# Kernel tuning notes

Measured on AMD Instinct MI355X. Metric: run time of the kernel, lower is better.

## Reference

```python
import jax, jax.numpy as jnp
import numpy as np
import math

NUM_HEADS = 16
HEAD_DIM = 64
EMBED = NUM_HEADS * HEAD_DIM  # 1024
T_FEAT = 128


def setup_inputs() -> dict:
    key = jax.random.key(0)
    ks = jax.random.split(key, 9)
    B, S = 4, 2048
    x = jax.random.normal(ks[0], (B, S, EMBED), dtype=jnp.float32)
    time_enc = jax.random.normal(ks[1], (B, T_FEAT), dtype=jnp.float32)
    s = 1.0 / math.sqrt(EMBED)
    Wq = jax.random.normal(ks[2], (EMBED, EMBED), dtype=jnp.float32) * s
    Wk = jax.random.normal(ks[3], (EMBED, EMBED), dtype=jnp.float32) * s
    Wv = jax.random.normal(ks[4], (EMBED, EMBED), dtype=jnp.float32) * s
    Wo = jax.random.normal(ks[5], (EMBED, EMBED), dtype=jnp.float32) * s
    bo = jnp.zeros((EMBED,), dtype=jnp.float32)
    Wt = jax.random.normal(ks[6], (T_FEAT, NUM_HEADS), dtype=jnp.float32) * (1.0 / math.sqrt(T_FEAT))
    bt = jnp.zeros((NUM_HEADS,), dtype=jnp.float32)
    return {"x": x, "time_enc": time_enc, "Wq": Wq, "Wk": Wk, "Wv": Wv,
            "Wo": Wo, "bo": bo, "Wt": Wt, "bt": bt}


def reference(x, time_enc, Wq, Wk, Wv, Wo, bo, Wt, bt):
    B, S, E = x.shape
    H, D = NUM_HEADS, HEAD_DIM
    scale = 1.0 / math.sqrt(D)
    # projections (no bias on q/k/v, bias on out)
    q = (x @ Wq).reshape(B, S, H, D).transpose(0, 2, 1, 3)  # [B,H,S,D]
    k = (x @ Wk).reshape(B, S, H, D).transpose(0, 2, 1, 3)
    v = (x @ Wv).reshape(B, S, H, D).transpose(0, 2, 1, 3)
    scores = jnp.einsum('bhqd,bhkd->bhqk', q, k) * scale
    # time-dependent per-head weighting (softmax over heads)
    time_weights = jax.nn.softmax(time_enc @ Wt + bt)  # [B,H]
    scores = scores * time_weights.reshape(B, H, 1, 1)
    attn = jax.nn.softmax(scores, axis=-1)
    out = jnp.einsum('bhqk,bhkd->bhqd', attn, v)
    out = out.transpose(0, 2, 1, 3).reshape(B, S, E)
    return out @ Wo + bo
```

## Files before the change

kernel.cpp:

```cpp
#include <hip/hip_runtime.h>
#include <cstdint>
#include <cstddef>

#define EMB   1024
#define NH    16
#define HD    64
#define SEQ   2048
#define NB    4
#define MROWS 8192

typedef short short8 __attribute__((ext_vector_type(8)));
typedef float floatx4 __attribute__((ext_vector_type(4)));

__device__ __forceinline__ unsigned short f2bf(float f) {
  return (unsigned short)((__float_as_uint(f) + 0x8000u) >> 16);
}

__device__ __forceinline__ void load16_lds(const unsigned short* g, unsigned short* l) {
  __builtin_amdgcn_global_load_lds((const __attribute__((address_space(1))) void*)g,
                                   (__attribute__((address_space(3))) void*)l, 16, 0, 0);
}

__global__ void time_weights_kernel(const float* __restrict__ te, const float* __restrict__ Wt,
                                    const float* __restrict__ bt, float* __restrict__ tw) {
  int t = threadIdx.x;
  int b = t >> 4, h = t & 15;
  float acc = bt[h];
  for (int i = 0; i < 128; i++) acc += te[b * 128 + i] * Wt[i * 16 + h];
  float m = acc;
  for (int off = 1; off < 16; off <<= 1) m = fmaxf(m, __shfl_xor(m, off, 16));
  float e = __expf(acc - m);
  float s = e;
  for (int off = 1; off < 16; off <<= 1) s += __shfl_xor(s, off, 16);
  tw[t] = (e / s) * 0.125f * 1.4426950408889634f;
}

__global__ void convert_x_kernel(const float4* __restrict__ x, unsigned short* __restrict__ out) {
  int i = blockIdx.x * blockDim.x + threadIdx.x;
  float4 v = x[i];
  unsigned int u0 = __float_as_uint(v.x) + 0x8000u, u1 = __float_as_uint(v.y) + 0x8000u;
  unsigned int u2 = __float_as_uint(v.z) + 0x8000u, u3 = __float_as_uint(v.w) + 0x8000u;
  uint2 p;
  p.x = (u0 >> 16) | (u1 & 0xffff0000u);
  p.y = (u2 >> 16) | (u3 & 0xffff0000u);
  *(uint2*)&out[(size_t)i * 4] = p;
}

__global__ void transpose_convert4_kernel(const float* __restrict__ Wq, const float* __restrict__ Wk,
                                          const float* __restrict__ Wv, const float* __restrict__ Wo,
                                          unsigned short* __restrict__ wqkvt, unsigned short* __restrict__ wot) {
  __shared__ float tile[32][33];
  int z = blockIdx.z;
  const float* W = (z == 0) ? Wq : (z == 1) ? Wk : (z == 2) ? Wv : Wo;
  unsigned short* out = (z < 3) ? (wqkvt + (size_t)z * EMB * EMB) : wot;
  int k0 = blockIdx.x * 32;
  int n0 = blockIdx.y * 32;
  int tx = threadIdx.x;
  int ty = threadIdx.y;
#pragma unroll
  for (int i = 0; i < 4; i++) {
    int k = ty + i * 8;
    tile[k][tx] = W[(size_t)(k0 + k) * EMB + n0 + tx];
  }
  __syncthreads();
#pragma unroll
  for (int i = 0; i < 4; i++) {
    int n = ty + i * 8;
    out[(size_t)(n0 + n) * EMB + k0 + tx] = f2bf(tile[tx][n]);
  }
}

template <int EPI>
__global__ __launch_bounds__(256) void gemm_kernel(
    const unsigned short* __restrict__ A, const unsigned short* __restrict__ Bt,
    unsigned short* __restrict__ qo, unsigned short* __restrict__ ko, unsigned short* __restrict__ vto,
    float* __restrict__ outf, const float* __restrict__ bias, const float* __restrict__ tw) {
  __shared__ unsigned short As[128 * 64];
  __shared__ unsigned short Bs[128 * 64];

  int tid = threadIdx.x;
  int lane = tid & 63, wid = tid >> 6;
  int quad = lane >> 4, l16 = lane & 15;
  int wm = wid >> 1, wn = wid & 1;
  int m0 = blockIdx.y * 128, n0 = blockIdx.x * 128;

  const unsigned short* gA[4];
  const unsigned short* gB[4];
  unsigned short* lA[4];
  unsigned short* lB[4];
#pragma unroll
  for (int c = 0; c < 4; c++) {
    int row = wid * 32 + c * 8 + (lane >> 3);
    int gcol = ((lane & 7) ^ (row & 7)) * 8;
    gA[c] = A + (size_t)(m0 + row) * 1024 + gcol;
    gB[c] = Bt + (size_t)(n0 + row) * 1024 + gcol;
    lA[c] = &As[(wid * 32 + c * 8) * 64];
    lB[c] = &Bs[(wid * 32 + c * 8) * 64];
  }

  int aoff[2];
#pragma unroll
  for (int kk = 0; kk < 2; kk++) aoff[kk] = (((kk * 4 + quad) ^ (l16 & 7)) * 8);

  floatx4 acc[4][4];
#pragma unroll
  for (int mi = 0; mi < 4; mi++)
#pragma unroll
    for (int ni = 0; ni < 4; ni++)
#pragma unroll
      for (int r = 0; r < 4; r++) acc[mi][ni][r] = 0.f;

  for (int k0 = 0; k0 < 1024; k0 += 64) {
    __syncthreads();
#pragma unroll
    for (int c = 0; c < 4; c++) {
      load16_lds(gA[c] + k0, lA[c]);
      load16_lds(gB[c] + k0, lB[c]);
    }
    asm volatile("s_waitcnt vmcnt(0) lgkmcnt(0)" ::: "memory");
    __syncthreads();

#pragma unroll
    for (int kk = 0; kk < 2; kk++) {
      short8 a_frag[4], b_frag[4];
#pragma unroll
      for (int mi = 0; mi < 4; mi++)
        a_frag[mi] = *(const short8*)&As[(wm * 64 + mi * 16 + l16) * 64 + aoff[kk]];
#pragma unroll
      for (int ni = 0; ni < 4; ni++)
        b_frag[ni] = *(const short8*)&Bs[(wn * 64 + ni * 16 + l16) * 64 + aoff[kk]];
#pragma unroll
      for (int mi = 0; mi < 4; mi++)
#pragma unroll
        for (int ni = 0; ni < 4; ni++)
          acc[mi][ni] = __builtin_amdgcn_mfma_f32_16x16x32_bf16(a_frag[mi], b_frag[ni], acc[mi][ni], 0, 0, 0);
    }
  }

#pragma unroll
  for (int mi = 0; mi < 4; mi++)
#pragma unroll
    for (int ni = 0; ni < 4; ni++)
#pragma unroll
      for (int r = 0; r < 4; r++) {
        int m = m0 + wm * 64 + mi * 16 + quad * 4 + r;
        int n = n0 + wn * 64 + ni * 16 + l16;
        float val = acc[mi][ni][r];
        if (EPI == 0) {
          int b = m >> 11, s = m & 2047;
          int proj = n >> 10, rem = n & 1023, hh = rem >> 6, d = rem & 63;
          size_t bh = (size_t)(b * NH + hh);
          if (proj == 0)      qo[(bh * SEQ + s) * HD + d] = f2bf(val * tw[bh]);
          else if (proj == 1) ko[(bh * SEQ + s) * HD + d] = f2bf(val);
          else                vto[(bh * HD + d) * SEQ + s] = f2bf(val);
        } else {
          outf[(size_t)m * EMB + n] = val + bias[n];
        }
      }
}

__global__ __launch_bounds__(256, 4) void attn_kernel(
    const unsigned short* __restrict__ qg, const unsigned short* __restrict__ kg,
    const unsigned short* __restrict__ vtg, unsigned short* __restrict__ aog) {
  __shared__ unsigned short Ks[64 * 64];
  __shared__ unsigned short Vs[64 * 64];
  __shared__ unsigned short Ps[4 * 2048];

  int tid = threadIdx.x;
  int lane = tid & 63, wid = tid >> 6;
  int quad = lane >> 4, l16 = lane & 15, l7 = lane & 7;
  int qt = blockIdx.x, h = blockIdx.y, b = blockIdx.z;
  int bh = b * NH + h;
  const unsigned short* qbase = qg + (size_t)bh * SEQ * HD + (size_t)qt * 128 * HD;
  const unsigned short* kbase = kg + (size_t)bh * SEQ * HD;
  const unsigned short* vbase = vtg + (size_t)bh * HD * SEQ;

  short8 b_q[2][2];
#pragma unroll
  for (int mi = 0; mi < 2; mi++)
#pragma unroll
    for (int kk = 0; kk < 2; kk++)
      b_q[mi][kk] = *(const short8*)&qbase[(wid * 32 + mi * 16 + l16) * 64 + kk * 32 + quad * 8];

  const unsigned short* gK[2];
  const unsigned short* gV[2];
  unsigned short* lK[2];
  unsigned short* lV[2];
#pragma unroll
  for (int c = 0; c < 2; c++) {
    int row = wid * 16 + c * 8 + (lane >> 3);
    int gcol = ((lane & 7) ^ (row & 7)) * 8;
    gK[c] = kbase + row * 64 + gcol;
    gV[c] = vbase + (size_t)row * SEQ + gcol;
    lK[c] = &Ks[(wid * 16 + c * 8) * 64];
    lV[c] = &Vs[(wid * 16 + c * 8) * 64];
  }

  int pg[2];
#pragma unroll
  for (int i = 0; i < 2; i++) pg[i] = l16 * 64 + (((i * 4 + quad) ^ l7) * 8);

  int wbase = wid * 2048;
  int chunkx = l16 & 14;
  int pwa[4];
#pragma unroll
  for (int ni = 0; ni < 4; ni++)
    pwa[ni] = wbase + l16 * 64 + (((ni * 4 + quad) ^ chunkx) * 4);
  int pra[2];
#pragma unroll
  for (int kk2 = 0; kk2 < 2; kk2++)
    pra[kk2] = wbase + l16 * 64 + (((kk2 * 8 + quad * 2) ^ chunkx) * 4);

  floatx4 O[4][2];
  float lsum[2] = {0.f, 0.f};
#pragma unroll
  for (int di = 0; di < 4; di++)
#pragma unroll
    for (int mi = 0; mi < 2; mi++)
#pragma unroll
      for (int r = 0; r < 4; r++) O[di][mi][r] = 0.f;

  for (int kb = 0; kb < 32; kb++) {
    __syncthreads();
#pragma unroll
    for (int c = 0; c < 2; c++) {
      load16_lds(gK[c] + kb * 4096, lK[c]);
      load16_lds(gV[c] + kb * 64, lV[c]);
    }
    asm volatile("s_waitcnt vmcnt(0) lgkmcnt(0)" ::: "memory");
    __syncthreads();

    floatx4 st[4][2];
#pragma unroll
    for (int ni = 0; ni < 4; ni++)
#pragma unroll
      for (int mi = 0; mi < 2; mi++)
#pragma unroll
        for (int r = 0; r < 4; r++) st[ni][mi][r] = 0.f;
#pragma unroll
    for (int kk = 0; kk < 2; kk++)
#pragma unroll
      for (int ni = 0; ni < 4; ni++) {
        short8 a_k = *(const short8*)&Ks[ni * 1024 + pg[kk]];
#pragma unroll
        for (int mi = 0; mi < 2; mi++)
          st[ni][mi] = __builtin_amdgcn_mfma_f32_16x16x32_bf16(a_k, b_q[mi][kk], st[ni][mi], 0, 0, 0);
      }

#pragma unroll
    for (int mi = 0; mi < 2; mi++)
#pragma unroll
      for (int ni = 0; ni < 4; ni++) {
        float p0 = __builtin_amdgcn_exp2f(st[ni][mi][0]);
        float p1 = __builtin_amdgcn_exp2f(st[ni][mi][1]);
        float p2 = __builtin_amdgcn_exp2f(st[ni][mi][2]);
        float p3 = __builtin_amdgcn_exp2f(st[ni][mi][3]);
        lsum[mi] += (p0 + p1) + (p2 + p3);
        unsigned int u0 = __float_as_uint(p0) + 0x8000u, u1 = __float_as_uint(p1) + 0x8000u;
        unsigned int u2 = __float_as_uint(p2) + 0x8000u, u3 = __float_as_uint(p3) + 0x8000u;
        uint2 w;
        w.x = (u0 >> 16) | (u1 & 0xffff0000u);
        w.y = (u2 >> 16) | (u3 & 0xffff0000u);
        *(uint2*)&Ps[pwa[ni] + mi * 1024] = w;
      }
    asm volatile("s_waitcnt lgkmcnt(0)" ::: "memory");

#pragma unroll
    for (int kk2 = 0; kk2 < 2; kk2++) {
      short8 av[4], bp[2];
#pragma unroll
      for (int di = 0; di < 4; di++)
        av[di] = *(const short8*)&Vs[di * 1024 + pg[kk2]];
#pragma unroll
      for (int mi = 0; mi < 2; mi++)
        bp[mi] = *(const short8*)&Ps[pra[kk2] + mi * 1024];
#pragma unroll
      for (int di = 0; di < 4; di++)
#pragma unroll
        for (int mi = 0; mi < 2; mi++)
          O[di][mi] = __builtin_amdgcn_mfma_f32_16x16x32_bf16(av[di], bp[mi], O[di][mi], 0, 0, 0);
    }
  }

  float inv[2];
#pragma unroll
  for (int mi = 0; mi < 2; mi++) {
    lsum[mi] += __shfl_xor(lsum[mi], 16);
    lsum[mi] += __shfl_xor(lsum[mi], 32);
    inv[mi] = 1.0f / lsum[mi];
  }

#pragma unroll
  for (int mi = 0; mi < 2; mi++) {
    int s = qt * 128 + wid * 32 + mi * 16 + l16;
    size_t rowbase = ((size_t)(b * SEQ + s) * NH + h) * HD;
#pragma unroll
    for (int di = 0; di < 4; di++) {
      unsigned int u0 = __float_as_uint(O[di][mi][0] * inv[mi]) + 0x8000u;
      unsigned int u1 = __float_as_uint(O[di][mi][1] * inv[mi]) + 0x8000u;
      unsigned int u2 = __float_as_uint(O[di][mi][2] * inv[mi]) + 0x8000u;
      unsigned int u3 = __float_as_uint(O[di][mi][3] * inv[mi]) + 0x8000u;
      uint2 w;
      w.x = (u0 >> 16) | (u1 & 0xffff0000u);
      w.y = (u2 >> 16) | (u3 & 0xffff0000u);
      *(uint2*)&aog[rowbase + di * 16 + quad * 4] = w;
    }
  }
}

extern "C" void kernel_launch(void* const* d_in, const int* in_sizes, int n_in,
                              void* d_out, int out_size, void* d_ws, size_t ws_size,
                              hipStream_t stream) {
  (void)in_sizes; (void)n_in; (void)out_size; (void)ws_size;
  const float* x  = (const float*)d_in[0];
  const float* te = (const float*)d_in[1];
  const float* Wq = (const float*)d_in[2];
  const float* Wk = (const float*)d_in[3];
  const float* Wv = (const float*)d_in[4];
  const float* Wo = (const float*)d_in[5];
  const float* bo = (const float*)d_in[6];
  const float* Wt = (const float*)d_in[7];
  const float* bt = (const float*)d_in[8];
  float* out = (float*)d_out;

  char* ws = (char*)d_ws;
  size_t off = 0;
  auto carve = [&](size_t bytes) -> void* {
    void* p = ws + off;
    off += (bytes + 255) & ~(size_t)255;
    return p;
  };
  float* twb            = (float*)carve(64 * sizeof(float));
  unsigned short* xb    = (unsigned short*)carve((size_t)MROWS * EMB * 2);
  unsigned short* wqkvt = (unsigned short*)carve((size_t)3 * EMB * EMB * 2);
  unsigned short* wot   = (unsigned short*)carve((size_t)EMB * EMB * 2);
  unsigned short* vtb   = (unsigned short*)carve((size_t)MROWS * EMB * 2);
  unsigned short* qb    = (unsigned short*)d_out;
  unsigned short* kb    = (unsigned short*)d_out + (size_t)MROWS * EMB;
  unsigned short* ao    = xb;

  time_weights_kernel<<<dim3(1), dim3(64), 0, stream>>>(te, Wt, bt, twb);
  convert_x_kernel<<<dim3(8192), dim3(256), 0, stream>>>((const float4*)x, xb);
  transpose_convert4_kernel<<<dim3(32, 32, 4), dim3(32, 8), 0, stream>>>(Wq, Wk, Wv, Wo, wqkvt, wot);
  gemm_kernel<0><<<dim3(24, 64), dim3(256), 0, stream>>>(xb, wqkvt, qb, kb, vtb, nullptr, nullptr, twb);
  attn_kernel<<<dim3(16, NH, NB), dim3(256), 0, stream>>>(qb, kb, vtb, ao);
  gemm_kernel<1><<<dim3(8, 64), dim3(256), 0, stream>>>(ao, wot, nullptr, nullptr, nullptr, out, bo, nullptr);
}
```

Before: 322.8 us.

## Restructure GEMM to 256x256 double-buffered tiles with workgroup swizzle

The projection GEMMs move from 128x128 tiles with 256 threads to 256x256 tiles with 512 threads and BK=32. Global-to-LDS loads are double buffered so the next K chunk is fetched while MFMAs run on the current one. The change also adds an XCD-aware workgroup index swizzle, raises MFMA priority with setprio, and writes V^T with packed 8-byte stores. Risks are higher register pressure from 32 accumulators per thread, and fewer blocks (384 and 128) on a GPU with 256 CUs, which may leave the output GEMM underfilled.

```diff
diff --git a/kernel.cpp b/kernel.cpp
--- a/kernel.cpp
+++ b/kernel.cpp
@@ -71,92 +71,139 @@
 }
 
 template <int EPI>
-__global__ __launch_bounds__(256) void gemm_kernel(
+__global__ __launch_bounds__(512, 2) void gemm_kernel(
     const unsigned short* __restrict__ A, const unsigned short* __restrict__ Bt,
     unsigned short* __restrict__ qo, unsigned short* __restrict__ ko, unsigned short* __restrict__ vto,
     float* __restrict__ outf, const float* __restrict__ bias, const float* __restrict__ tw) {
-  __shared__ unsigned short As[128 * 64];
-  __shared__ unsigned short Bs[128 * 64];
-
-  int tid = threadIdx.x;
-  int lane = tid & 63, wid = tid >> 6;
-  int quad = lane >> 4, l16 = lane & 15;
-  int wm = wid >> 1, wn = wid & 1;
-  int m0 = blockIdx.y * 128, n0 = blockIdx.x * 128;
-
-  const unsigned short* gA[4];
-  const unsigned short* gB[4];
-  unsigned short* lA[4];
-  unsigned short* lB[4];
-#pragma unroll
-  for (int c = 0; c < 4; c++) {
-    int row = wid * 32 + c * 8 + (lane >> 3);
-    int gcol = ((lane & 7) ^ (row & 7)) * 8;
-    gA[c] = A + (size_t)(m0 + row) * 1024 + gcol;
-    gB[c] = Bt + (size_t)(n0 + row) * 1024 + gcol;
-    lA[c] = &As[(wid * 32 + c * 8) * 64];
-    lB[c] = &Bs[(wid * 32 + c * 8) * 64];
-  }
-
-  int aoff[2];
-#pragma unroll
-  for (int kk = 0; kk < 2; kk++) aoff[kk] = (((kk * 4 + quad) ^ (l16 & 7)) * 8);
-
-  floatx4 acc[4][4];
-#pragma unroll
-  for (int mi = 0; mi < 4; mi++)
+  __shared__ unsigned short ldsu[32768];
+
+  const int tid = threadIdx.x;
+  const int lane = tid & 63, wid = tid >> 6;
+  const int quad = lane >> 4, l16 = lane & 15;
+  const int wm = wid >> 2, wn = wid & 3;
+
+  const int gx = gridDim.x;
+  const int nwg = gx * gridDim.y;
+  const int fid = blockIdx.y * gx + blockIdx.x;
+  const int swzid = (fid & 7) * (nwg >> 3) + (fid >> 3);
+  const int m0 = (swzid / gx) * 256;
+  const int n0 = (swzid % gx) * 256;
+
+  const int trow = tid >> 2;
+  const int sw = (((tid & 3) ^ ((tid >> 2) & 3) ^ ((tid >> 4) & 3))) * 8;
+  const unsigned short* gA0 = A + (size_t)(m0 + trow) * 1024 + sw;
+  const unsigned short* gA1 = A + (size_t)(m0 + 128 + trow) * 1024 + sw;
+  const unsigned short* gB0 = Bt + (size_t)(n0 + trow) * 1024 + sw;
+  const unsigned short* gB1 = Bt + (size_t)(n0 + 128 + trow) * 1024 + sw;
+  unsigned short* lds_w = ldsu + (wid << 9);
+
+  const int swl = (l16 & 3) ^ (l16 >> 2);
+  const int foff = (quad ^ swl) * 8;
+  const int abase = (wm * 128 + l16) * 32 + foff;
+  const int bbase = 8192 + (wn * 64 + l16) * 32 + foff;
+
+  floatx4 acc[8][4];
+#pragma unroll
+  for (int mi = 0; mi < 8; mi++)
 #pragma unroll
     for (int ni = 0; ni < 4; ni++)
 #pragma unroll
       for (int r = 0; r < 4; r++) acc[mi][ni][r] = 0.f;
 
-  for (int k0 = 0; k0 < 1024; k0 += 64) {
-    __syncthreads();
-#pragma unroll
-    for (int c = 0; c < 4; c++) {
-      load16_lds(gA[c] + k0, lA[c]);
-      load16_lds(gB[c] + k0, lB[c]);
+  load16_lds(gA0, lds_w);
+  load16_lds(gA1, lds_w + 4096);
+  load16_lds(gB0, lds_w + 8192);
+  load16_lds(gB1, lds_w + 12288);
+
+  for (int t = 0; t < 32; ++t) {
+    const int cur = (t & 1) << 14;
+    const int nxt = ((t + 1) & 1) << 14;
+    const int kc = ((t + 1) & 31) * 32;
+    load16_lds(gA0 + kc, lds_w + nxt);
+    load16_lds(gA1 + kc, lds_w + nxt + 4096);
+    load16_lds(gB0 + kc, lds_w + nxt + 8192);
+    load16_lds(gB1 + kc, lds_w + nxt + 12288);
+    asm volatile("s_waitcnt vmcnt(4)" ::: "memory");
+    asm volatile("s_barrier" ::: "memory");
+
+    short8 af[8], bf[4];
+#pragma unroll
+    for (int mi = 0; mi < 8; mi++) af[mi] = *(const short8*)&ldsu[cur + abase + mi * 512];
+#pragma unroll
+    for (int ni = 0; ni < 4; ni++) bf[ni] = *(const short8*)&ldsu[cur + bbase + ni * 512];
+    __builtin_amdgcn_s_setprio(1);
+#pragma unroll
+    for (int mi = 0; mi < 8; mi++)
+#pragma unroll
+      for (int ni = 0; ni < 4; ni++)
+        acc[mi][ni] = __builtin_amdgcn_mfma_f32_16x16x32_bf16(af[mi], bf[ni], acc[mi][ni], 0, 0, 0);
+    __builtin_amdgcn_s_setprio(0);
+    asm volatile("s_barrier" ::: "memory");
+  }
+  asm volatile("s_waitcnt vmcnt(0)" ::: "memory");
+
+  if (EPI == 1) {
+#pragma unroll
+    for (int mi = 0; mi < 8; mi++)
+#pragma unroll
+      for (int ni = 0; ni < 4; ni++) {
+        const int n = n0 + wn * 64 + ni * 16 + l16;
+        const float bs = bias[n];
+        const int mb = m0 + wm * 128 + mi * 16 + quad * 4;
+#pragma unroll
+        for (int r = 0; r < 4; r++)
+          outf[(size_t)(mb + r) * EMB + n] = acc[mi][ni][r] + bs;
+      }
+  } else {
+    const int proj = n0 >> 10;
+    const int b = m0 >> 11;
+    const int hw = ((n0 + wn * 64) >> 6) & 15;
+    const size_t bh = (size_t)b * NH + hw;
+    const int mbase = m0 + wm * 128;
+    if (proj == 0) {
+      const float tws = tw[bh];
+#pragma unroll
+      for (int mi = 0; mi < 8; mi++) {
+        const int s = ((mbase + mi * 16) & 2047) + quad * 4;
+#pragma unroll
+        for (int ni = 0; ni < 4; ni++) {
+          const int d = ni * 16 + l16;
+          unsigned short* qp = qo + (bh * SEQ + s) * HD + d;
+#pragma unroll
+          for (int r = 0; r < 4; r++) qp[(size_t)r * HD] = f2bf(acc[mi][ni][r] * tws);
+        }
+      }
+    } else if (proj == 1) {
+#pragma unroll
+      for (int mi = 0; mi < 8; mi++) {
+        const int s = ((mbase + mi * 16) & 2047) + quad * 4;
+#pragma unroll
+        for (int ni = 0; ni < 4; ni++) {
+          const int d = ni * 16 + l16;
+          unsigned short* kp = ko + (bh * SEQ + s) * HD + d;
+#pragma unroll
+          for (int r = 0; r < 4; r++) kp[(size_t)r * HD] = f2bf(acc[mi][ni][r]);
+        }
+      }
+    } else {
+#pragma unroll
+      for (int mi = 0; mi < 8; mi++) {
+        const int s = ((mbase + mi * 16) & 2047) + quad * 4;
+#pragma unroll
+        for (int ni = 0; ni < 4; ni++) {
+          const int d = ni * 16 + l16;
+          unsigned int u0 = __float_as_uint(acc[mi][ni][0]) + 0x8000u;
+          unsigned int u1 = __float_as_uint(acc[mi][ni][1]) + 0x8000u;
+          unsigned int u2 = __float_as_uint(acc[mi][ni][2]) + 0x8000u;
+          unsigned int u3 = __float_as_uint(acc[mi][ni][3]) + 0x8000u;
+          uint2 w;
+          w.x = (u0 >> 16) | (u1 & 0xffff0000u);
+          w.y = (u2 >> 16) | (u3 & 0xffff0000u);
+          *(uint2*)&vto[(bh * HD + d) * SEQ + s] = w;
+        }
+      }
     }
-    asm volatile("s_waitcnt vmcnt(0) lgkmcnt(0)" ::: "memory");
-    __syncthreads();
-
-#pragma unroll
-    for (int kk = 0; kk < 2; kk++) {
-      short8 a_frag[4], b_frag[4];
-#pragma unroll
-      for (int mi = 0; mi < 4; mi++)
-        a_frag[mi] = *(const short8*)&As[(wm * 64 + mi * 16 + l16) * 64 + aoff[kk]];
-#pragma unroll
-      for (int ni = 0; ni < 4; ni++)
-        b_frag[ni] = *(const short8*)&Bs[(wn * 64 + ni * 16 + l16) * 64 + aoff[kk]];
-#pragma unroll
-      for (int mi = 0; mi < 4; mi++)
-#pragma unroll
-        for (int ni = 0; ni < 4; ni++)
-          acc[mi][ni] = __builtin_amdgcn_mfma_f32_16x16x32_bf16(a_frag[mi], b_frag[ni], acc[mi][ni], 0, 0, 0);
-    }
-  }
-
-#pragma unroll
-  for (int mi = 0; mi < 4; mi++)
-#pragma unroll
-    for (int ni = 0; ni < 4; ni++)
-#pragma unroll
-      for (int r = 0; r < 4; r++) {
-        int m = m0 + wm * 64 + mi * 16 + quad * 4 + r;
-        int n = n0 + wn * 64 + ni * 16 + l16;
-        float val = acc[mi][ni][r];
-        if (EPI == 0) {
-          int b = m >> 11, s = m & 2047;
-          int proj = n >> 10, rem = n & 1023, hh = rem >> 6, d = rem & 63;
-          size_t bh = (size_t)(b * NH + hh);
-          if (proj == 0)      qo[(bh * SEQ + s) * HD + d] = f2bf(val * tw[bh]);
-          else if (proj == 1) ko[(bh * SEQ + s) * HD + d] = f2bf(val);
-          else                vto[(bh * HD + d) * SEQ + s] = f2bf(val);
-        } else {
-          outf[(size_t)m * EMB + n] = val + bias[n];
-        }
-      }
+  }
 }
 
 __global__ __launch_bounds__(256, 4) void attn_kernel(
@@ -342,7 +389,7 @@
   time_weights_kernel<<<dim3(1), dim3(64), 0, stream>>>(te, Wt, bt, twb);
   convert_x_kernel<<<dim3(8192), dim3(256), 0, stream>>>((const float4*)x, xb);
   transpose_convert4_kernel<<<dim3(32, 32, 4), dim3(32, 8), 0, stream>>>(Wq, Wk, Wv, Wo, wqkvt, wot);
-  gemm_kernel<0><<<dim3(24, 64), dim3(256), 0, stream>>>(xb, wqkvt, qb, kb, vtb, nullptr, nullptr, twb);
+  gemm_kernel<0><<<dim3(12, 32), dim3(512), 0, stream>>>(xb, wqkvt, qb, kb, vtb, nullptr, nullptr, twb);
   attn_kernel<<<dim3(16, NH, NB), dim3(256), 0, stream>>>(qb, kb, vtb, ao);
-  gemm_kernel<1><<<dim3(8, 64), dim3(256), 0, stream>>>(ao, wot, nullptr, nullptr, nullptr, out, bo, nullptr);
-}
+  gemm_kernel<1><<<dim3(4, 32), dim3(512), 0, stream>>>(ao, wot, nullptr, nullptr, nullptr, out, bo, nullptr);
+}
```

Result: faster. 302.3 us (-6.3%).
